# Kernel tuning notes

Hardware: AMD Instinct MI355X
Metric: run time of the kernel (lower is better)

## Reference

```python
import jax, jax.numpy as jnp
import numpy as np

N = 100000   # nodes
E = 200000   # edges
G = 2000     # graphs
D = 300      # emb_dim
L = 5        # layers
FEAT = 512
MAX_DEGREE = 4
EPS = 1e-5


def setup_inputs() -> dict:
    key = jax.random.key(0)
    ks = jax.random.split(key, 24)
    atom_vocab = jnp.array([119, 3, 11, 9, 7, 4, 6, 2, 2])
    bond_vocab = jnp.array([4, 3, 2])  # keep type < 4 so self-loop type 4 is distinct
    x = jax.random.randint(ks[0], (N, 9), 0, 1 << 30) % atom_vocab
    edge_index = jax.random.randint(ks[1], (2, E), 0, N)
    edge_attr = jax.random.randint(ks[2], (E, 3), 0, 1 << 30) % bond_vocab
    edge_distance = jax.random.uniform(ks[3], (E,), dtype=jnp.float32) * 4.0
    batch = jnp.sort(jax.random.randint(ks[4], (N,), 0, G))
    nrm = lambda k, s, sc: (jax.random.normal(k, s, dtype=jnp.float32) * sc)
    return {
        "x": x, "edge_index": edge_index, "edge_attr": edge_attr,
        "edge_distance": edge_distance, "batch": batch,
        "atom_emb": nrm(ks[5], (9, 119, D), 0.1),
        "att_vec": nrm(ks[6], (D,), 1.0),
        "out_lin_w": nrm(ks[7], (D, D), 0.05), "out_lin_b": jnp.zeros((D,)),
        "g_means": jax.random.uniform(ks[8], (D,), minval=2.0, maxval=3.0),
        "g_stds": jax.random.uniform(ks[9], (D,), minval=1.0, maxval=1.5),
        "scale_param": jnp.full((MAX_DEGREE, D), np.log(0.1), dtype=jnp.float32),
        "edge_emb": nrm(ks[10], (L, 3, 5, D), 0.1),
        "mlp_w1": nrm(ks[11], (L, D, 2 * D), 0.05), "mlp_b1": jnp.zeros((L, 2 * D)),
        "mlp_w2": nrm(ks[12], (L, 2 * D, D), 0.05), "mlp_b2": jnp.zeros((L, D)),
        "bn_gamma": jnp.ones((L, D)), "bn_beta": jnp.zeros((L, D)),
        "feat_w": nrm(ks[13], (D, FEAT), 0.05), "feat_b": jnp.zeros((FEAT,)),
        "ol_w1": nrm(ks[14], (FEAT, FEAT), 0.05), "ol_b1": jnp.zeros((FEAT,)),
        "ol_w2": nrm(ks[15], (FEAT, FEAT // 2), 0.05), "ol_b2": jnp.zeros((FEAT // 2,)),
    }


def reference(x, edge_index, edge_attr, edge_distance, batch,
              atom_emb, att_vec, out_lin_w, out_lin_b, g_means, g_stds, scale_param,
              edge_emb, mlp_w1, mlp_b1, mlp_w2, mlp_b2, bn_gamma, bn_beta,
              feat_w, feat_b, ol_w1, ol_b1, ol_w2, ol_b2):
    src, dst = edge_index[0], edge_index[1]
    # node degree from incoming edges, clamped as in the torch code
    counts = jax.ops.segment_sum(jnp.ones((E,), jnp.int32), dst, num_segments=N)
    node_degree = jnp.clip(counts - 1, 0, MAX_DEGREE - 1)
    # GaussianLayer on edge distances -> [E, D]
    std = jnp.abs(g_stds) + 0.01
    a = (2.0 * 3.14159) ** 0.5
    z = (edge_distance[:, None] - g_means[None, :]) / std[None, :]
    g = jnp.exp(-0.5 * z * z) / (a * std[None, :])
    h_in = jax.ops.segment_sum(g, dst, num_segments=N)          # [N, D]
    h_in = jnp.exp(scale_param)[node_degree] * h_in             # ScaleDegreeLayer
    # AtomEncoderAttention: [N, 9, D] embeddings fused by softmax attention
    embs = atom_emb[jnp.arange(9)[None, :], x]                  # [N, 9, D]
    scores = jnp.einsum('nfd,d->nf', embs, att_vec)
    w = jax.nn.softmax(scores, axis=1)
    fused = jnp.einsum('nfd,nf->nd', embs, w)
    h = fused @ out_lin_w + out_lin_b + h_in
    # self-loop augmented edges (same for every layer)
    loop = jnp.arange(N)
    src_a = jnp.concatenate([src, loop])
    dst_a = jnp.concatenate([dst, loop])
    loop_attr = jnp.tile(jnp.array([[4, 0, 0]], edge_attr.dtype), (N, 1))
    attr_a = jnp.concatenate([edge_attr, loop_attr], axis=0)    # [E+N, 3]
    for l in range(L):
        e = (edge_emb[l, 0][attr_a[:, 0]] + edge_emb[l, 1][attr_a[:, 1]]
             + edge_emb[l, 2][attr_a[:, 2]])                     # [E+N, D]
        msg = h[src_a] + e
        agg = jax.ops.segment_sum(msg, dst_a, num_segments=N)
        h = jax.nn.relu(agg @ mlp_w1[l] + mlp_b1[l]) @ mlp_w2[l] + mlp_b2[l]
        mu = h.mean(axis=0)
        var = jnp.mean((h - mu) ** 2, axis=0)
        h = bn_gamma[l] * (h - mu) * jax.lax.rsqrt(var + EPS) + bn_beta[l]
        if l < L - 1:
            h = jax.nn.relu(h)
    # global mean pool
    sums = jax.ops.segment_sum(h, batch, num_segments=G)
    cnt = jax.ops.segment_sum(jnp.ones((N,), h.dtype), batch, num_segments=G)
    hg = sums / jnp.maximum(cnt, 1.0)[:, None]
    h_feat = hg @ feat_w + feat_b                                # [G, 512]
    out = jax.nn.relu(h_feat @ ol_w1 + ol_b1) @ ol_w2 + ol_b2    # [G, 256]
    return (h_feat, out)
```

## Files before the change

kernel.cpp:

```cpp
#include <hip/hip_runtime.h>
#include <hip/hip_bf16.h>


#define NN   100000
#define EE   200000
#define GG   2000
#define DD   300
#define D2   600
#define LL   5
#define FEATN 512
#define OUT2 256
#define ROWS_PER 256
#define RPB  48
#define MLP_LDS (RPB * 632 * 2)

typedef __hip_bfloat16 bf16;
typedef short vec8s __attribute__((ext_vector_type(8)));
typedef short vec4s __attribute__((ext_vector_type(4)));
typedef float vec4f __attribute__((ext_vector_type(4)));

__device__ __forceinline__ short f2bs(float v) {
    bf16 h = __float2bfloat16(v);
    return __builtin_bit_cast(short, h);
}
__device__ __forceinline__ float bs2f(short s) {
    unsigned u = ((unsigned)(unsigned short)s) << 16;
    return __builtin_bit_cast(float, u);
}

__global__ void k_pack(const float* __restrict__ src0, short* __restrict__ dst0,
                       int Ksrc, int Nsrc, int KT, int NPAD,
                       size_t sstride, size_t dstride)
{
    const float* src = src0 + (size_t)blockIdx.y * sstride;
    short* dst = dst0 + (size_t)blockIdx.y * dstride;
    int idx = blockIdx.x * 256 + threadIdx.x;
    int total = KT * NPAD * 32;
    if (idx >= total) return;
    int col = idx % NPAD;
    int tmp = idx / NPAD;
    int kk  = tmp % 32;
    int kt  = tmp / 32;
    int k = kt * 32 + kk;
    short v = 0;
    if (k < Ksrc && col < Nsrc) v = f2bs(src[(size_t)k * Nsrc + col]);
    dst[((size_t)kt * NPAD + col) * 32 + kk] = v;
}

__global__ void k_etab(const float* __restrict__ edge_emb, float* __restrict__ E)
{
    int i = blockIdx.x * 256 + threadIdx.x;
    if (i >= LL * 25 * DD) return;
    int d = i % DD;
    int t = i / DD;
    int c = t % 25;
    int l = t / 25;
    int a0 = (c == 24) ? 4 : (c / 6);
    int a1 = (c == 24) ? 0 : ((c % 6) / 2);
    int a2 = (c == 24) ? 0 : (c % 2);
    const float* e0 = edge_emb + (size_t)((l * 3 + 0) * 5) * DD;
    const float* e1 = edge_emb + (size_t)((l * 3 + 1) * 5) * DD;
    const float* e2 = edge_emb + (size_t)((l * 3 + 2) * 5) * DD;
    E[i] = e0[a0 * DD + d] + e1[a1 * DD + d] + e2[a2 * DD + d];
}

__global__ void k_repack(int* __restrict__ eidx, const int* __restrict__ src,
                         const int* __restrict__ attr)
{
    int i = blockIdx.x * 256 + threadIdx.x;
    if (i >= EE) return;
    int e = eidx[i];
    int c = attr[e * 3] * 6 + attr[e * 3 + 1] * 2 + attr[e * 3 + 2];
    eidx[i] = src[e] | (c << 17);
}

__global__ __launch_bounds__(512, 4) void k_mlp2(
    const short* __restrict__ Qb, const short* __restrict__ W1P,
    const float* __restrict__ b1, const short* __restrict__ W2P,
    const float* __restrict__ b2, void* __restrict__ Pout, int f16out,
    float* __restrict__ RS)
{
    extern __shared__ __align__(16) char smem_c[];
    short* Apan = (short*)smem_c;
    short (*Hl)[632] = (short(*)[632])smem_c;

    const int t = threadIdx.x;
    const int wv = t >> 6, lane = t & 63;
    const int m = lane & 15, quad = lane >> 4;
    const int rb = (int)blockIdx.x * RPB;
    const int rep = ((int)blockIdx.x & 31) * 600;

    {
        const short* qbase = Qb + (size_t)rb * 320;
#pragma unroll
        for (int i = 0; i < 4; i++) {
            int j = i * 8 + wv;
            if (j < 30) {
                int c   = j * 64 + lane;
                int c8  = c >> 3;
                int row = c8 / 5;
                int ch  = (c8 - row * 5) * 8 + (lane & 7);
                const short* src = qbase + (size_t)row * 320
                                 + (size_t)((ch ^ (row & 7)) * 8);
                __builtin_amdgcn_global_load_lds(
                    (const __attribute__((address_space(1))) unsigned int*)src,
                    (__attribute__((address_space(3))) unsigned int*)(smem_c + j * 1024),
                    16, 0, 0);
            }
        }
    }

    const int ql   = quad ^ (m & 3);
    const int eh   = (m >> 2) & 1;
    const int abE  = m * 320 + ql * 8 + eh * 32;
    const int abO  = m * 320 + ql * 8 + (1 - eh) * 32;

    vec4f acc1[3][5];
#pragma unroll
    for (int g = 0; g < 3; g++)
#pragma unroll
        for (int cf = 0; cf < 5; cf++) acc1[g][cf] = (vec4f)0.f;

    const short* w1b = W1P + ((size_t)(wv * 80 + m) * 32) + quad * 8;
    vec8s bcur[5], bnxt[5];
#pragma unroll
    for (int cf = 0; cf < 5; cf++) bcur[cf] = *(const vec8s*)(w1b + cf * 512);

    __syncthreads();

#pragma unroll
    for (int kt = 0; kt < 10; kt++) {
        if (kt < 9) {
            const short* wn = w1b + (size_t)(kt + 1) * 20480;
#pragma unroll
            for (int cf = 0; cf < 5; cf++) bnxt[cf] = *(const vec8s*)(wn + cf * 512);
        }
        const int base = (kt & 1) ? abO : abE;
        const int koff = (kt & ~1) * 32;
        vec8s af[3];
#pragma unroll
        for (int g = 0; g < 3; g++)
            af[g] = *(const vec8s*)(Apan + base + koff + g * 5120);
        __builtin_amdgcn_s_setprio(1);
#pragma unroll
        for (int cf = 0; cf < 5; cf++)
#pragma unroll
            for (int g = 0; g < 3; g++)
                acc1[g][cf] = __builtin_amdgcn_mfma_f32_16x16x32_bf16(
                    bcur[cf], af[g], acc1[g][cf], 0, 0, 0);
        __builtin_amdgcn_s_setprio(0);
#pragma unroll
        for (int cf = 0; cf < 5; cf++) bcur[cf] = bnxt[cf];
    }

    const short* w2b = W2P + ((size_t)(wv * 48 + m) * 32) + quad * 8;
    vec8s b2f[2][3];
#pragma unroll
    for (int cf = 0; cf < 3; cf++) {
        b2f[0][cf] = *(const vec8s*)(w2b + cf * 512);
        b2f[1][cf] = *(const vec8s*)(w2b + 12288 + cf * 512);
    }

    __syncthreads();

#pragma unroll
    for (int g = 0; g < 3; g++) {
#pragma unroll
        for (int cf = 0; cf < 5; cf++) {
            const int col0 = wv * 80 + cf * 16 + quad * 4;
            if (col0 < 600) {
                vec4f bv = *(const vec4f*)(b1 + col0);
                vec4s o;
#pragma unroll
                for (int r = 0; r < 4; r++)
                    o[r] = f2bs(fmaxf(acc1[g][cf][r] + bv[r], 0.f));
                *(vec4s*)&Hl[g * 16 + m][col0] = o;
            } else if (col0 < 608) {
                *(vec4s*)&Hl[g * 16 + m][col0] = (vec4s)0;
            }
        }
    }
    __syncthreads();

    {
        vec4f acc2[3][3];
#pragma unroll
        for (int g = 0; g < 3; g++)
#pragma unroll
            for (int cf = 0; cf < 3; cf++) acc2[g][cf] = (vec4f)0.f;

#pragma unroll
        for (int kt = 0; kt < 19; kt++) {
            vec8s ha[3];
#pragma unroll
            for (int g = 0; g < 3; g++)
                ha[g] = *(const vec8s*)&Hl[g * 16 + m][kt * 32 + quad * 8];
            __builtin_amdgcn_s_setprio(1);
#pragma unroll
            for (int cf = 0; cf < 3; cf++)
#pragma unroll
                for (int g = 0; g < 3; g++)
                    acc2[g][cf] = __builtin_amdgcn_mfma_f32_16x16x32_bf16(
                        ha[g], b2f[kt & 1][cf], acc2[g][cf], 0, 0, 0);
            __builtin_amdgcn_s_setprio(0);
            if (kt < 17) {
                const short* wn = w2b + (size_t)(kt + 2) * 12288;
#pragma unroll
                for (int cf = 0; cf < 3; cf++)
                    b2f[kt & 1][cf] = *(const vec8s*)(wn + cf * 512);
            }
        }

#pragma unroll
        for (int cf = 0; cf < 3; cf++) {
            int gc = wv * 48 + cf * 16 + m;
            bool ok = (gc < DD);
            float bv = ok ? b2[gc] : 0.f;
            float s = 0.f, q = 0.f;
#pragma unroll
            for (int g = 0; g < 3; g++) {
#pragma unroll
                for (int reg = 0; reg < 4; reg++) {
                    int row = rb + g * 16 + quad * 4 + reg;
                    bool vr = row < NN;
                    float v = acc2[g][cf][reg] + bv;
                    if (ok && vr) {
                        if (f16out)
                            ((short*)Pout)[(size_t)row * 300 + gc] = f2bs(v);
                        else
                            ((float*)Pout)[(size_t)row * DD + gc] = v;
                    }
                    if (vr) { s += v; q += v * v; }
                }
            }
            s += __shfl_xor(s, 16); s += __shfl_xor(s, 32);
            q += __shfl_xor(q, 16); q += __shfl_xor(q, 32);
            if (ok && quad == 0) {
                atomicAdd(&RS[rep + gc], s);
                atomicAdd(&RS[19200 + rep + gc], q);
            }
        }
    }
}

__global__ __launch_bounds__(256) void k_g1(
    const short* __restrict__ Qb, const short* __restrict__ WP,
    const float* __restrict__ bias, float* __restrict__ H)
{
    const int t = threadIdx.x;
    const int wv = t >> 6, lane = t & 63;
    const int m = lane & 15, quad = lane >> 4;
    const int rb = (int)blockIdx.x * 32;
    const short* arow0 = Qb + (size_t)(rb + m) * 320 + quad * 8;
    const short* arow1 = arow0 + (size_t)16 * 320;
    const short* wb0 = WP + ((size_t)(wv * 80 + m) * 32) + quad * 8;

    vec4f acc[2][5];
#pragma unroll
    for (int g = 0; g < 2; g++)
#pragma unroll
        for (int cf = 0; cf < 5; cf++) acc[g][cf] = (vec4f)0.f;

    vec8s af0 = *(const vec8s*)arow0;
    vec8s af1 = *(const vec8s*)arow1;
    vec8s bcur[5], bnxt[5];
#pragma unroll
    for (int cf = 0; cf < 5; cf++) bcur[cf] = *(const vec8s*)(wb0 + cf * 512);

#pragma unroll
    for (int kt = 0; kt < 10; kt++) {
        vec8s an0 = af0, an1 = af1;
        if (kt < 9) {
            an0 = *(const vec8s*)(arow0 + (kt + 1) * 32);
            an1 = *(const vec8s*)(arow1 + (kt + 1) * 32);
            const short* wn = wb0 + (size_t)(kt + 1) * 12288;
#pragma unroll
            for (int cf = 0; cf < 5; cf++) bnxt[cf] = *(const vec8s*)(wn + cf * 512);
        }
#pragma unroll
        for (int cf = 0; cf < 5; cf++) {
            acc[0][cf] = __builtin_amdgcn_mfma_f32_16x16x32_bf16(af0, bcur[cf], acc[0][cf], 0, 0, 0);
            acc[1][cf] = __builtin_amdgcn_mfma_f32_16x16x32_bf16(af1, bcur[cf], acc[1][cf], 0, 0, 0);
        }
        af0 = an0; af1 = an1;
#pragma unroll
        for (int cf = 0; cf < 5; cf++) bcur[cf] = bnxt[cf];
    }
#pragma unroll
    for (int cf = 0; cf < 5; cf++) {
        int gc = wv * 80 + cf * 16 + m;
        if (gc >= DD) continue;
        float bv = bias[gc];
#pragma unroll
        for (int g = 0; g < 2; g++)
#pragma unroll
            for (int reg = 0; reg < 4; reg++)
                H[(size_t)(rb + g * 16 + quad * 4 + reg) * DD + gc] = acc[g][cf][reg] + bv;
    }
}

__global__ void k_degree(const int* __restrict__ dst, int* __restrict__ deg) {
    int e = blockIdx.x * 256 + threadIdx.x;
    if (e < EE) atomicAdd(&deg[dst[e]], 1);
}

__global__ void k_scan1(const int* __restrict__ deg, int* __restrict__ off,
                        int* __restrict__ bsum)
{
    __shared__ int s[256];
    int i = blockIdx.x * 256 + threadIdx.x;
    int v = (i < NN) ? deg[i] : 0;
    s[threadIdx.x] = v;
    __syncthreads();
    for (int o = 1; o < 256; o <<= 1) {
        int tv = (threadIdx.x >= o) ? s[threadIdx.x - o] : 0;
        __syncthreads();
        s[threadIdx.x] += tv;
        __syncthreads();
    }
    if (i < NN) off[i] = s[threadIdx.x] - v;
    if (threadIdx.x == 255) bsum[blockIdx.x] = s[255];
}

__global__ void k_scan2(int* __restrict__ bsum, int* __restrict__ off, int nb) {
    __shared__ int ws[8];
    int t = threadIdx.x;
    int v = (t < nb) ? bsum[t] : 0;
    int s = v;
    for (int o = 1; o < 64; o <<= 1) {
        int u = __shfl_up(s, o, 64);
        if ((t & 63) >= o) s += u;
    }
    if ((t & 63) == 63) ws[t >> 6] = s;
    __syncthreads();
    if (t < 8) {
        int a = ws[t];
        for (int o = 1; o < 8; o <<= 1) {
            int u = __shfl_up(a, o, 64);
            if (t >= o) a += u;
        }
        ws[t] = a;
    }
    __syncthreads();
    int base = (t >> 6) ? ws[(t >> 6) - 1] : 0;
    int incl = s + base;
    if (t < nb) bsum[t] = incl - v;
    if (t == nb - 1) off[NN] = incl;
}

__global__ void k_scan3(int* __restrict__ off, const int* __restrict__ bsum,
                        int* __restrict__ curs)
{
    int i = blockIdx.x * 256 + threadIdx.x;
    if (i >= NN) return;
    int v = off[i] + bsum[i >> 8];
    off[i] = v;
    curs[i] = v;
}

__global__ void k_fill(const int* __restrict__ dst, int* __restrict__ curs,
                       int* __restrict__ eidx)
{
    int e = blockIdx.x * 256 + threadIdx.x;
    if (e >= EE) return;
    int pos = atomicAdd(&curs[dst[e]], 1);
    eidx[pos] = e;
}

__global__ __launch_bounds__(256) void k_embed(
    const int* __restrict__ x, const float* __restrict__ atom_emb,
    const float* __restrict__ att_vec, short* __restrict__ fusedb)
{
    int wave = threadIdx.x >> 6;
    int lane = threadIdx.x & 63;
    int n = blockIdx.x * 4 + wave;
    if (n >= NN) return;

    float att[5];
#pragma unroll
    for (int j = 0; j < 5; j++) {
        int d = lane + 64 * j;
        att[j] = (d < DD) ? att_vec[d] : 0.f;
    }
    float emb[9][5];
    float sc[9];
#pragma unroll
    for (int f = 0; f < 9; f++) {
        int idx = x[n * 9 + f];
        const float* p = atom_emb + (size_t)(f * 119 + idx) * DD;
        float partial = 0.f;
#pragma unroll
        for (int j = 0; j < 5; j++) {
            int d = lane + 64 * j;
            float v = (d < DD) ? p[d] : 0.f;
            emb[f][j] = v;
            partial += v * att[j];
        }
#pragma unroll
        for (int off = 32; off; off >>= 1) partial += __shfl_xor(partial, off, 64);
        sc[f] = partial;
    }
    float mx = sc[0];
#pragma unroll
    for (int f = 1; f < 9; f++) mx = fmaxf(mx, sc[f]);
    float s = 0.f;
#pragma unroll
    for (int f = 0; f < 9; f++) { sc[f] = __expf(sc[f] - mx); s += sc[f]; }
    float inv = 1.f / s;
#pragma unroll
    for (int j = 0; j < 5; j++) {
        int d = lane + 64 * j;
        float acc = 0.f;
        if (d < DD) {
#pragma unroll
            for (int f = 0; f < 9; f++) acc += emb[f][j] * sc[f];
            acc *= inv;
        }
        fusedb[(size_t)n * 320 + d] = (d < DD) ? f2bs(acc) : (short)0;
    }
}

__global__ __launch_bounds__(320) void k_gaussg(
    const int* __restrict__ off, const int* __restrict__ eidx,
    const float* __restrict__ dist, const float* __restrict__ g_means,
    const float* __restrict__ g_stds, const float* __restrict__ scale_p,
    float* __restrict__ H)
{
    int n = blockIdx.x;
    int d = threadIdx.x;
    if (d >= DD) return;
    int beg = off[n], end = off[n + 1];
    if (beg == end) return;
    float sd = fabsf(g_stds[d]) + 0.01f;
    float mean = g_means[d];
    float inv_asd = 1.f / (2.5066263f * sd);
    float sum = 0.f;
    float xv = dist[eidx[beg]];
    for (int i = beg; i < end; i++) {
        float xn = 0.f;
        if (i + 1 < end) xn = dist[eidx[i + 1]];
        float z = (xv - mean) / sd;
        sum += __expf(-0.5f * z * z) * inv_asd;
        xv = xn;
    }
    int deg = end - beg;
    int c = deg - 1; c = c < 0 ? 0 : (c > 3 ? 3 : c);
    H[(size_t)n * DD + d] += __expf(scale_p[c * DD + d]) * sum;
}

__global__ __launch_bounds__(320) void k_agg(
    const void* __restrict__ P, const int* __restrict__ off,
    const int* __restrict__ eidxp, const float* __restrict__ E,
    const float* __restrict__ scale, const float* __restrict__ shift,
    int apply, short* __restrict__ Qb)
{
    int tn = threadIdx.x / 80;
    int td = threadIdx.x - tn * 80;
    int n = blockIdx.x * 4 + tn;
    if (n >= NN) return;
    int d4 = td * 4;
    if (d4 >= DD) {
        *(vec4s*)&Qb[(size_t)n * 320 + d4] = (vec4s)0;
        return;
    }
    const float* Pf = (const float*)P;
    const short* Ph = (const short*)P;

    float a[4];
    float sc[4], sh[4];
    if (apply) {
        vec4f s4 = *(const vec4f*)(scale + d4);
        vec4f h4 = *(const vec4f*)(shift + d4);
#pragma unroll
        for (int j = 0; j < 4; j++) { sc[j] = s4[j]; sh[j] = h4[j]; }
        vec4s pv = *(const vec4s*)(Ph + (size_t)n * 300 + d4);
#pragma unroll
        for (int j = 0; j < 4; j++)
            a[j] = fmaxf(bs2f(pv[j]) * sc[j] + sh[j], 0.f);
    } else {
        vec4f self = *(const vec4f*)(Pf + (size_t)n * DD + d4);
#pragma unroll
        for (int j = 0; j < 4; j++) a[j] = self[j];
    }
    {
        vec4f es = *(const vec4f*)(E + 24 * DD + d4);
#pragma unroll
        for (int j = 0; j < 4; j++) a[j] += es[j];
    }

    int beg = off[n], end = off[n + 1];
    if (beg < end) {
        int v0 = eidxp[beg];
        int v1 = (beg + 1 < end) ? eidxp[beg + 1] : 0;
        if (apply) {
            int s0 = v0 & 131071, c0 = v0 >> 17;
            vec4s pc = *(const vec4s*)(Ph + (size_t)s0 * 300 + d4);
            vec4f ec = *(const vec4f*)(E + c0 * DD + d4);
            for (int i = beg; i < end; i++) {
                int v2 = (i + 2 < end) ? eidxp[i + 2] : 0;
                vec4s pn = (vec4s)0;
                vec4f en = (vec4f)0.f;
                if (i + 1 < end) {
                    int s1 = v1 & 131071, c1 = v1 >> 17;
                    pn = *(const vec4s*)(Ph + (size_t)s1 * 300 + d4);
                    en = *(const vec4f*)(E + c1 * DD + d4);
                }
#pragma unroll
                for (int j = 0; j < 4; j++)
                    a[j] += fmaxf(bs2f(pc[j]) * sc[j] + sh[j], 0.f) + ec[j];
                pc = pn; ec = en;
                v0 = v1; v1 = v2;
            }
        } else {
            int s0 = v0 & 131071, c0 = v0 >> 17;
            vec4f pc = *(const vec4f*)(Pf + (size_t)s0 * DD + d4);
            vec4f ec = *(const vec4f*)(E + c0 * DD + d4);
            for (int i = beg; i < end; i++) {
                int v2 = (i + 2 < end) ? eidxp[i + 2] : 0;
                vec4f pn = (vec4f)0.f;
                vec4f en = (vec4f)0.f;
                if (i + 1 < end) {
                    int s1 = v1 & 131071, c1 = v1 >> 17;
                    pn = *(const vec4f*)(Pf + (size_t)s1 * DD + d4);
                    en = *(const vec4f*)(E + c1 * DD + d4);
                }
#pragma unroll
                for (int j = 0; j < 4; j++) a[j] += pc[j] + ec[j];
                pc = pn; ec = en;
                v0 = v1; v1 = v2;
            }
        }
    }
    vec4s o;
#pragma unroll
    for (int j = 0; j < 4; j++) o[j] = f2bs(a[j]);
    *(vec4s*)&Qb[(size_t)n * 320 + d4] = o;
}

__global__ void k_bnprep(const float* __restrict__ RS, float* __restrict__ SC,
                         const float* __restrict__ gamma,
                         const float* __restrict__ beta)
{
    int d = threadIdx.x + blockIdx.x * 256;
    if (d >= DD) return;
    float s = 0.f, q = 0.f;
    for (int r = 0; r < 32; r++) {
        s += RS[r * 600 + d];
        q += RS[19200 + r * 600 + d];
    }
    float mu = s * (1.f / NN);
    float var = q * (1.f / NN) - mu * mu;
    var = fmaxf(var, 0.f);
    float sc = gamma[d] * rsqrtf(var + 1e-5f);
    SC[d] = sc;
    SC[600 + d] = beta[d] - mu * sc;
}

__global__ __launch_bounds__(320) void k_pool(const float* __restrict__ H,
                                              const int* __restrict__ batch,
                                              float* __restrict__ HG,
                                              float* __restrict__ cnt)
{
    __shared__ int sb[ROWS_PER];
    int r0 = blockIdx.x * ROWS_PER;
    int rend = min(r0 + ROWS_PER, NN);
    for (int i = threadIdx.x; i < rend - r0; i += 320) sb[i] = batch[r0 + i];
    __syncthreads();
    int d = threadIdx.x;
    if (d >= DD) return;
    int cur = sb[0];
    float acc = 0.f;
    int run = 0;
    for (int r = r0; r < rend; r++) {
        int b = sb[r - r0];
        if (b != cur) {
            atomicAdd(&HG[(size_t)cur * DD + d], acc);
            if (d == 0) atomicAdd(&cnt[cur], (float)run);
            acc = 0.f; run = 0; cur = b;
        }
        acc += H[(size_t)r * DD + d];
        run++;
    }
    atomicAdd(&HG[(size_t)cur * DD + d], acc);
    if (d == 0) atomicAdd(&cnt[cur], (float)run);
}

__global__ void k_hgdiv(float* __restrict__ HG, const float* __restrict__ cnt,
                        const float* __restrict__ SC)
{
    int idx = blockIdx.x * 256 + threadIdx.x;
    if (idx >= GG * DD) return;
    int d = idx % DD;
    float mean = HG[idx] / fmaxf(cnt[idx / DD], 1.0f);
    HG[idx] = mean * SC[d] + SC[600 + d];
}

__global__ __launch_bounds__(256) void k_gemm(
    const float* __restrict__ A, const float* __restrict__ W,
    const float* __restrict__ bias, float* __restrict__ Cf,
    float* __restrict__ Cout, int M, int K, int Ncol, int relu)
{
    __shared__ float Ash[16][33];
    const int tx = threadIdx.x & 15;
    const int ty = threadIdx.x >> 4;
    const int rb = blockIdx.y * 16;
    const int col = blockIdx.x * 64 + tx * 4;

    float acc[4] = {0.f, 0.f, 0.f, 0.f};

    for (int k0 = 0; k0 < K; k0 += 32) {
        {
            int r  = threadIdx.x >> 4;
            int kk = (threadIdx.x & 15) * 2;
            int row = rb + r;
            float vx = 0.f, vy = 0.f;
            if (row < M) {
                const float* ap = A + (size_t)row * K + k0 + kk;
                if (k0 + kk + 1 < K) {
                    float2 v = *(const float2*)ap;
                    vx = v.x; vy = v.y;
                } else if (k0 + kk < K) {
                    vx = ap[0];
                }
            }
            Ash[r][kk]     = vx;
            Ash[r][kk + 1] = vy;
        }
        __syncthreads();

        const int kmax = (K - k0 < 32) ? (K - k0) : 32;
        const float* wp = W + (size_t)k0 * Ncol + col;
#pragma unroll 4
        for (int k = 0; k < kmax; k++) {
            float4 wv = *(const float4*)(wp + (size_t)k * Ncol);
            float a = Ash[ty][k];
            acc[0] += a * wv.x; acc[1] += a * wv.y;
            acc[2] += a * wv.z; acc[3] += a * wv.w;
        }
        __syncthreads();
    }

    int row = rb + ty;
    if (row < M) {
        float4 bv = *(const float4*)(bias + col);
        float4 o;
        o.x = acc[0] + bv.x; o.y = acc[1] + bv.y;
        o.z = acc[2] + bv.z; o.w = acc[3] + bv.w;
        if (relu) {
            o.x = fmaxf(o.x, 0.f); o.y = fmaxf(o.y, 0.f);
            o.z = fmaxf(o.z, 0.f); o.w = fmaxf(o.w, 0.f);
        }
        if (Cf)   *(float4*)(Cf   + (size_t)row * Ncol + col) = o;
        if (Cout) *(float4*)(Cout + (size_t)row * Ncol + col) = o;
    }
}

extern "C" void kernel_launch(void* const* d_in, const int* in_sizes, int n_in,
                              void* d_out, int out_size, void* d_ws, size_t ws_size,
                              hipStream_t stream)
{
    const int*   x          = (const int*)  d_in[0];
    const int*   edge_index = (const int*)  d_in[1];
    const int*   edge_attr  = (const int*)  d_in[2];
    const float* edge_dist  = (const float*)d_in[3];
    const int*   batch      = (const int*)  d_in[4];
    const float* atom_emb   = (const float*)d_in[5];
    const float* att_vec    = (const float*)d_in[6];
    const float* out_lin_w  = (const float*)d_in[7];
    const float* out_lin_b  = (const float*)d_in[8];
    const float* g_means    = (const float*)d_in[9];
    const float* g_stds     = (const float*)d_in[10];
    const float* scale_p    = (const float*)d_in[11];
    const float* edge_emb   = (const float*)d_in[12];
    const float* mlp_w1     = (const float*)d_in[13];
    const float* mlp_b1     = (const float*)d_in[14];
    const float* mlp_w2     = (const float*)d_in[15];
    const float* mlp_b2     = (const float*)d_in[16];
    const float* bn_gamma   = (const float*)d_in[17];
    const float* bn_beta    = (const float*)d_in[18];
    const float* feat_w     = (const float*)d_in[19];
    const float* feat_b     = (const float*)d_in[20];
    const float* ol_w1      = (const float*)d_in[21];
    const float* ol_b1      = (const float*)d_in[22];
    const float* ol_w2      = (const float*)d_in[23];
    const float* ol_b2      = (const float*)d_in[24];
    (void)in_sizes; (void)n_in; (void)out_size; (void)ws_size;

    const int* srcp = edge_index;
    const int* dstp = edge_index + EE;

    char* ws = (char*)d_ws;
    size_t off_b = 0;
    auto alloc = [&](size_t bytes) -> char* {
        char* p = ws + off_b;
        off_b += (bytes + 255) & ~(size_t)255;
        return p;
    };
    float* H     = (float*)alloc((size_t)NN * DD * 4 + 256);
    float* AGG   = (float*)alloc((size_t)NN * DD * 4 + 256);
    int*   DEG   = (int*)  alloc((size_t)NN * 4);
    float* CNT   = (float*)alloc(GG * 4);
    float* HG    = (float*)alloc((size_t)GG * DD * 4);
    float* HFEAT = (float*)alloc((size_t)GG * FEATN * 4);
    float* TMP   = (float*)alloc((size_t)GG * FEATN * 4);

    short* OLWP = (short*)HG;
    short* W1P  = OLWP + (size_t)10 * 384 * 32;
    short* W2P  = W1P + (size_t)LL * 10 * 640 * 32;
    char*  csr  = (char*)(W2P + (size_t)LL * 19 * 384 * 32);
    int*   OFF  = (int*)csr;
    int*   CURS = (int*)(csr + 400128);
    int*   EIDX = (int*)(csr + 800128);
    float* ETAB = (float*)(csr + 1600256);
    float* REPS = (float*)(csr + 1750272);
    float* SCL  = (float*)(csr + 2518528);
    int*   BSUM = (int*)CNT;

    float* outp = (float*)d_out;

    hipFuncSetAttribute((const void*)k_mlp2,
                        hipFuncAttributeMaxDynamicSharedMemorySize, MLP_LDS);

    k_pack<<<dim3(480, 1), 256, 0, stream>>>(out_lin_w, OLWP, 300, 300, 10, 384,
                                             0, 0);
    k_pack<<<dim3(800, LL), 256, 0, stream>>>(mlp_w1, W1P, DD, D2, 10, 640,
                                              (size_t)DD * D2, (size_t)10 * 640 * 32);
    k_pack<<<dim3(912, LL), 256, 0, stream>>>(mlp_w2, W2P, D2, DD, 19, 384,
                                              (size_t)D2 * DD, (size_t)19 * 384 * 32);
    k_etab<<<(LL * 25 * DD + 255) / 256, 256, 0, stream>>>(edge_emb, ETAB);
    hipMemsetAsync(REPS, 0, (size_t)LL * 2 * 32 * 600 * 4, stream);

    hipMemsetAsync(DEG, 0, (size_t)NN * 4, stream);
    k_degree<<<(EE + 255) / 256, 256, 0, stream>>>(dstp, DEG);
    k_scan1<<<391, 256, 0, stream>>>(DEG, OFF, BSUM);
    k_scan2<<<1, 512, 0, stream>>>(BSUM, OFF, 391);
    k_scan3<<<391, 256, 0, stream>>>(OFF, BSUM, CURS);
    k_fill<<<(EE + 255) / 256, 256, 0, stream>>>(dstp, CURS, EIDX);

    short* QB = (short*)AGG;
    k_embed<<<(NN + 3) / 4, 256, 0, stream>>>(x, atom_emb, att_vec, QB);
    k_g1<<<NN / 32, 256, 0, stream>>>(QB, OLWP, out_lin_b, H);
    k_gaussg<<<NN, 320, 0, stream>>>(OFF, EIDX, edge_dist, g_means, g_stds,
                                     scale_p, H);
    k_repack<<<(EE + 255) / 256, 256, 0, stream>>>(EIDX, srcp, edge_attr);

    for (int l = 0; l < LL; l++) {
        const float* sc = SCL + (size_t)(l - 1) * 1200;
        k_agg<<<(NN + 3) / 4, 320, 0, stream>>>(
            (const void*)H, OFF, EIDX, ETAB + (size_t)l * 25 * DD,
            l > 0 ? sc : SCL, l > 0 ? sc + 600 : SCL, l > 0 ? 1 : 0, QB);
        k_mlp2<<<(NN + RPB - 1) / RPB, 512, MLP_LDS, stream>>>(
            QB, W1P + (size_t)l * 10 * 640 * 32, mlp_b1 + (size_t)l * D2,
            W2P + (size_t)l * 19 * 384 * 32, mlp_b2 + (size_t)l * DD,
            (void*)H, (l < LL - 1) ? 1 : 0,
            REPS + (size_t)l * 38400);
        k_bnprep<<<2, 256, 0, stream>>>(REPS + (size_t)l * 38400,
                                        SCL + (size_t)l * 1200,
                                        bn_gamma + (size_t)l * DD,
                                        bn_beta + (size_t)l * DD);
    }

    hipMemsetAsync(CNT, 0, (size_t)GG * 4, stream);
    hipMemsetAsync(HG, 0, (size_t)GG * DD * 4, stream);
    k_pool<<<(NN + ROWS_PER - 1) / ROWS_PER, 320, 0, stream>>>(H, batch, HG, CNT);
    k_hgdiv<<<(GG * DD + 255) / 256, 256, 0, stream>>>(HG, CNT,
                                                       SCL + (size_t)4 * 1200);
    {
        dim3 grid((FEATN + 63) / 64, (GG + 15) / 16);
        k_gemm<<<grid, 256, 0, stream>>>(HG, feat_w, feat_b, HFEAT, outp,
                                         GG, DD, FEATN, 0);
    }
    {
        dim3 grid((FEATN + 63) / 64, (GG + 15) / 16);
        k_gemm<<<grid, 256, 0, stream>>>(HFEAT, ol_w1, ol_b1, TMP, nullptr,
                                         GG, FEATN, FEATN, 1);
    }
    {
        dim3 grid((OUT2 + 63) / 64, (GG + 15) / 16);
        k_gemm<<<grid, 256, 0, stream>>>(TMP, ol_w2, ol_b2, nullptr,
                                         outp + (size_t)GG * FEATN,
                                         GG, FEATN, OUT2, 0);
    }
}
```

Baseline: 1.792 ms.

## Fuse edge aggregation into MLP kernel prologue, ping-pong activation buffers

Removes the separate k_agg kernel and performs the gather-sum of neighbor messages directly inside k_mlp2, writing the bf16 aggregated rows straight into the swizzled LDS A-panel. The goal is to avoid writing and re-reading the intermediate QB buffer and to drop one launch per layer. Because the MLP now reads its input and writes its output in the same kernel, activations ping-pong between H and AGG, and pooling reads from AGG. In exchange, the fused prologue uses a simple non-prefetched gather loop and may lengthen the MLP kernel's critical path by adding irregular memory latency before the MFMA work.

```diff
diff --git a/kernel.cpp b/kernel.cpp
--- a/kernel.cpp
+++ b/kernel.cpp
@@ -12,7 +12,7 @@
 #define OUT2 256
 #define ROWS_PER 256
 #define RPB  48
-#define MLP_LDS (RPB * 632 * 2)
+#define MLP_LDS (RPB * 632 * 2 + 256)
 
 typedef __hip_bfloat16 bf16;
 typedef short vec8s __attribute__((ext_vector_type(8)));
@@ -75,14 +75,19 @@
 }
 
 __global__ __launch_bounds__(512, 4) void k_mlp2(
-    const short* __restrict__ Qb, const short* __restrict__ W1P,
-    const float* __restrict__ b1, const short* __restrict__ W2P,
-    const float* __restrict__ b2, void* __restrict__ Pout, int f16out,
+    const void* __restrict__ Pin, int aggmode,
+    const int* __restrict__ off, const int* __restrict__ eidxp,
+    const float* __restrict__ E,
+    const float* __restrict__ scale, const float* __restrict__ shift,
+    const short* __restrict__ W1P, const float* __restrict__ b1,
+    const short* __restrict__ W2P, const float* __restrict__ b2,
+    void* __restrict__ Pout, int f16out,
     float* __restrict__ RS)
 {
     extern __shared__ __align__(16) char smem_c[];
     short* Apan = (short*)smem_c;
     short (*Hl)[632] = (short(*)[632])smem_c;
+    int* sOff = (int*)(smem_c + RPB * 632 * 2);
 
     const int t = threadIdx.x;
     const int wv = t >> 6, lane = t & 63;
@@ -90,24 +95,66 @@
     const int rb = (int)blockIdx.x * RPB;
     const int rep = ((int)blockIdx.x & 31) * 600;
 
-    {
-        const short* qbase = Qb + (size_t)rb * 320;
-#pragma unroll
-        for (int i = 0; i < 4; i++) {
-            int j = i * 8 + wv;
-            if (j < 30) {
-                int c   = j * 64 + lane;
-                int c8  = c >> 3;
-                int row = c8 / 5;
-                int ch  = (c8 - row * 5) * 8 + (lane & 7);
-                const short* src = qbase + (size_t)row * 320
-                                 + (size_t)((ch ^ (row & 7)) * 8);
-                __builtin_amdgcn_global_load_lds(
-                    (const __attribute__((address_space(1))) unsigned int*)src,
-                    (__attribute__((address_space(3))) unsigned int*)(smem_c + j * 1024),
-                    16, 0, 0);
+    const short* w1b = W1P + ((size_t)(wv * 80 + m) * 32) + quad * 8;
+    vec8s bcur[5], bnxt[5];
+#pragma unroll
+    for (int cf = 0; cf < 5; cf++) bcur[cf] = *(const vec8s*)(w1b + cf * 512);
+
+    if (t < RPB + 1) {
+        int rr = rb + t;
+        sOff[t] = off[rr <= NN ? rr : NN];
+    }
+    __syncthreads();
+
+    const float* Pf = (const float*)Pin;
+    const short* Ph = (const short*)Pin;
+    for (int it = t; it < RPB * 80; it += 512) {
+        int r  = it / 80;
+        int cg = it - r * 80;
+        int d4 = cg * 4;
+        int li = r * 320 + (((d4 >> 3) ^ (r & 7)) * 8) + (d4 & 7);
+        int n = rb + r;
+        if (n >= NN || d4 >= DD) {
+            *(vec4s*)&Apan[li] = (vec4s)0;
+            continue;
+        }
+        float a[4];
+        int beg = sOff[r], end = sOff[r + 1];
+        if (aggmode) {
+            vec4f s4 = *(const vec4f*)(scale + d4);
+            vec4f h4 = *(const vec4f*)(shift + d4);
+            vec4s pv = *(const vec4s*)(Ph + (size_t)n * 300 + d4);
+            vec4f e24 = *(const vec4f*)(E + 24 * DD + d4);
+#pragma unroll
+            for (int j = 0; j < 4; j++)
+                a[j] = fmaxf(bs2f(pv[j]) * s4[j] + h4[j], 0.f) + e24[j];
+            for (int i = beg; i < end; i++) {
+                int v = eidxp[i];
+                int s = v & 131071, c = v >> 17;
+                vec4s pg = *(const vec4s*)(Ph + (size_t)s * 300 + d4);
+                vec4f ev = *(const vec4f*)(E + c * DD + d4);
+#pragma unroll
+                for (int j = 0; j < 4; j++)
+                    a[j] += fmaxf(bs2f(pg[j]) * s4[j] + h4[j], 0.f) + ev[j];
             }
-        }
+        } else {
+            vec4f pv = *(const vec4f*)(Pf + (size_t)n * DD + d4);
+            vec4f e24 = *(const vec4f*)(E + 24 * DD + d4);
+#pragma unroll
+            for (int j = 0; j < 4; j++) a[j] = pv[j] + e24[j];
+            for (int i = beg; i < end; i++) {
+                int v = eidxp[i];
+                int s = v & 131071, c = v >> 17;
+                vec4f pg = *(const vec4f*)(Pf + (size_t)s * DD + d4);
+                vec4f ev = *(const vec4f*)(E + c * DD + d4);
+#pragma unroll
+                for (int j = 0; j < 4; j++) a[j] += pg[j] + ev[j];
+            }
+        }
+        vec4s o;
+#pragma unroll
+        for (int j = 0; j < 4; j++) o[j] = f2bs(a[j]);
+        *(vec4s*)&Apan[li] = o;
     }
 
     const int ql   = quad ^ (m & 3);
@@ -120,11 +167,6 @@
     for (int g = 0; g < 3; g++)
 #pragma unroll
         for (int cf = 0; cf < 5; cf++) acc1[g][cf] = (vec4f)0.f;
-
-    const short* w1b = W1P + ((size_t)(wv * 80 + m) * 32) + quad * 8;
-    vec8s bcur[5], bnxt[5];
-#pragma unroll
-    for (int cf = 0; cf < 5; cf++) bcur[cf] = *(const vec8s*)(w1b + cf * 512);
 
     __syncthreads();
 
@@ -446,95 +488,6 @@
     int deg = end - beg;
     int c = deg - 1; c = c < 0 ? 0 : (c > 3 ? 3 : c);
     H[(size_t)n * DD + d] += __expf(scale_p[c * DD + d]) * sum;
-}
-
-__global__ __launch_bounds__(320) void k_agg(
-    const void* __restrict__ P, const int* __restrict__ off,
-    const int* __restrict__ eidxp, const float* __restrict__ E,
-    const float* __restrict__ scale, const float* __restrict__ shift,
-    int apply, short* __restrict__ Qb)
-{
-    int tn = threadIdx.x / 80;
-    int td = threadIdx.x - tn * 80;
-    int n = blockIdx.x * 4 + tn;
-    if (n >= NN) return;
-    int d4 = td * 4;
-    if (d4 >= DD) {
-        *(vec4s*)&Qb[(size_t)n * 320 + d4] = (vec4s)0;
-        return;
-    }
-    const float* Pf = (const float*)P;
-    const short* Ph = (const short*)P;
-
-    float a[4];
-    float sc[4], sh[4];
-    if (apply) {
-        vec4f s4 = *(const vec4f*)(scale + d4);
-        vec4f h4 = *(const vec4f*)(shift + d4);
-#pragma unroll
-        for (int j = 0; j < 4; j++) { sc[j] = s4[j]; sh[j] = h4[j]; }
-        vec4s pv = *(const vec4s*)(Ph + (size_t)n * 300 + d4);
-#pragma unroll
-        for (int j = 0; j < 4; j++)
-            a[j] = fmaxf(bs2f(pv[j]) * sc[j] + sh[j], 0.f);
-    } else {
-        vec4f self = *(const vec4f*)(Pf + (size_t)n * DD + d4);
-#pragma unroll
-        for (int j = 0; j < 4; j++) a[j] = self[j];
-    }
-    {
-        vec4f es = *(const vec4f*)(E + 24 * DD + d4);
-#pragma unroll
-        for (int j = 0; j < 4; j++) a[j] += es[j];
-    }
-
-    int beg = off[n], end = off[n + 1];
-    if (beg < end) {
-        int v0 = eidxp[beg];
-        int v1 = (beg + 1 < end) ? eidxp[beg + 1] : 0;
-        if (apply) {
-            int s0 = v0 & 131071, c0 = v0 >> 17;
-            vec4s pc = *(const vec4s*)(Ph + (size_t)s0 * 300 + d4);
-            vec4f ec = *(const vec4f*)(E + c0 * DD + d4);
-            for (int i = beg; i < end; i++) {
-                int v2 = (i + 2 < end) ? eidxp[i + 2] : 0;
-                vec4s pn = (vec4s)0;
-                vec4f en = (vec4f)0.f;
-                if (i + 1 < end) {
-                    int s1 = v1 & 131071, c1 = v1 >> 17;
-                    pn = *(const vec4s*)(Ph + (size_t)s1 * 300 + d4);
-                    en = *(const vec4f*)(E + c1 * DD + d4);
-                }
-#pragma unroll
-                for (int j = 0; j < 4; j++)
-                    a[j] += fmaxf(bs2f(pc[j]) * sc[j] + sh[j], 0.f) + ec[j];
-                pc = pn; ec = en;
-                v0 = v1; v1 = v2;
-            }
-        } else {
-            int s0 = v0 & 131071, c0 = v0 >> 17;
-            vec4f pc = *(const vec4f*)(Pf + (size_t)s0 * DD + d4);
-            vec4f ec = *(const vec4f*)(E + c0 * DD + d4);
-            for (int i = beg; i < end; i++) {
-                int v2 = (i + 2 < end) ? eidxp[i + 2] : 0;
-                vec4f pn = (vec4f)0.f;
-                vec4f en = (vec4f)0.f;
-                if (i + 1 < end) {
-                    int s1 = v1 & 131071, c1 = v1 >> 17;
-                    pn = *(const vec4f*)(Pf + (size_t)s1 * DD + d4);
-                    en = *(const vec4f*)(E + c1 * DD + d4);
-                }
-#pragma unroll
-                for (int j = 0; j < 4; j++) a[j] += pc[j] + ec[j];
-                pc = pn; ec = en;
-                v0 = v1; v1 = v2;
-            }
-        }
-    }
-    vec4s o;
-#pragma unroll
-    for (int j = 0; j < 4; j++) o[j] = f2bs(a[j]);
-    *(vec4s*)&Qb[(size_t)n * 320 + d4] = o;
 }
 
 __global__ void k_bnprep(const float* __restrict__ RS, float* __restrict__ SC,
@@ -746,13 +699,14 @@
 
     for (int l = 0; l < LL; l++) {
         const float* sc = SCL + (size_t)(l - 1) * 1200;
-        k_agg<<<(NN + 3) / 4, 320, 0, stream>>>(
-            (const void*)H, OFF, EIDX, ETAB + (size_t)l * 25 * DD,
-            l > 0 ? sc : SCL, l > 0 ? sc + 600 : SCL, l > 0 ? 1 : 0, QB);
+        const void* Pin  = (l & 1) ? (const void*)AGG : (const void*)H;
+        void*       Pout = (l & 1) ? (void*)H         : (void*)AGG;
         k_mlp2<<<(NN + RPB - 1) / RPB, 512, MLP_LDS, stream>>>(
-            QB, W1P + (size_t)l * 10 * 640 * 32, mlp_b1 + (size_t)l * D2,
+            Pin, l > 0 ? 1 : 0, OFF, EIDX, ETAB + (size_t)l * 25 * DD,
+            l > 0 ? sc : SCL, l > 0 ? sc + 600 : SCL,
+            W1P + (size_t)l * 10 * 640 * 32, mlp_b1 + (size_t)l * D2,
             W2P + (size_t)l * 19 * 384 * 32, mlp_b2 + (size_t)l * DD,
-            (void*)H, (l < LL - 1) ? 1 : 0,
+            Pout, (l < LL - 1) ? 1 : 0,
             REPS + (size_t)l * 38400);
         k_bnprep<<<2, 256, 0, stream>>>(REPS + (size_t)l * 38400,
                                         SCL + (size_t)l * 1200,
@@ -762,7 +716,7 @@
 
     hipMemsetAsync(CNT, 0, (size_t)GG * 4, stream);
     hipMemsetAsync(HG, 0, (size_t)GG * DD * 4, stream);
-    k_pool<<<(NN + ROWS_PER - 1) / ROWS_PER, 320, 0, stream>>>(H, batch, HG, CNT);
+    k_pool<<<(NN + ROWS_PER - 1) / ROWS_PER, 320, 0, stream>>>(AGG, batch, HG, CNT);
     k_hgdiv<<<(GG * DD + 255) / 256, 256, 0, stream>>>(HG, CNT,
                                                        SCL + (size_t)4 * 1200);
     {
```

After: 1.866 ms. 1.04x slower.
